# Performance work log

Measured on AMD Instinct MI355X. Metric: run time of the kernel, lower is better.

The kernel has to match this reference:

```python
import jax, jax.numpy as jnp
import numpy as np

N_HEAD = 16
D_HEAD = 64
D_MODEL = 1024
SCALE = 1.0 / float(D_HEAD) ** 0.5
LN_EPS = 1e-5


def _rel_shift(x):
    # x: [b, n, i, j] -> Transformer-XL relative shift
    b, n, i, j = x.shape
    x = jnp.pad(x, ((0, 0), (0, 0), (0, 0), (1, 0)))  # zero-pad front of last dim
    x = x.reshape(b, n, j + 1, i)[:, :, 1:, :]
    return x.reshape(b, n, i, j)


def _layer_norm(x, g, b):
    mu = jnp.mean(x, axis=-1, keepdims=True)
    var = jnp.mean(jnp.square(x - mu), axis=-1, keepdims=True)
    return g * (x - mu) / jnp.sqrt(var + LN_EPS) + b


def setup_inputs() -> dict:
    key = jax.random.key(0)
    ks = jax.random.split(key, 8)
    qlen, bsz = 1024, 4
    w = jax.random.normal(ks[0], (qlen, bsz, D_MODEL), jnp.float32)
    r = jax.random.normal(ks[1], (qlen, D_MODEL), jnp.float32)
    r_w_bias = 0.02 * jax.random.normal(ks[2], (N_HEAD, D_HEAD), jnp.float32)
    r_r_bias = 0.02 * jax.random.normal(ks[3], (N_HEAD, D_HEAD), jnp.float32)
    attn_mask = jnp.triu(jnp.ones((qlen, qlen), bool), 1)  # causal, True = masked
    qkv_w = 0.02 * jax.random.normal(ks[4], (D_MODEL, 3 * N_HEAD * D_HEAD), jnp.float32)
    qkv_b = jnp.zeros((3 * N_HEAD * D_HEAD,), jnp.float32)
    rk_w = 0.02 * jax.random.normal(ks[5], (D_MODEL, N_HEAD * D_HEAD), jnp.float32)
    rk_b = jnp.zeros((N_HEAD * D_HEAD,), jnp.float32)
    o_w = 0.02 * jax.random.normal(ks[6], (N_HEAD * D_HEAD, D_MODEL), jnp.float32)
    o_b = jnp.zeros((D_MODEL,), jnp.float32)
    ln_g = jnp.ones((D_MODEL,), jnp.float32)
    ln_b = jnp.zeros((D_MODEL,), jnp.float32)
    return {"w": w, "r": r, "r_w_bias": r_w_bias, "r_r_bias": r_r_bias,
            "qkv_w": qkv_w, "qkv_b": qkv_b, "rk_w": rk_w, "rk_b": rk_b,
            "o_w": o_w, "o_b": o_b, "ln_g": ln_g, "ln_b": ln_b,
            "attn_mask": attn_mask}


def reference(w, r, r_w_bias, r_r_bias, qkv_w, qkv_b, rk_w, rk_b, o_w, o_b, ln_g, ln_b, attn_mask):
    qlen, bsz, _ = w.shape
    # post-lnorm path (pre_lnorm=False)
    heads = w @ qkv_w + qkv_b                       # [q, b, 3*H*D]
    q, k, v = jnp.split(heads, 3, axis=-1)
    q = q.reshape(qlen, bsz, N_HEAD, D_HEAD)
    k = k.reshape(qlen, bsz, N_HEAD, D_HEAD)
    v = v.reshape(qlen, bsz, N_HEAD, D_HEAD)
    rk = (r @ rk_w + rk_b).reshape(-1, N_HEAD, D_HEAD)  # [rlen, H, D]
    AC = jnp.einsum('ibnd,jbnd->bnij', q + r_w_bias, k)
    BD = _rel_shift(jnp.einsum('ibnd,jnd->bnij', q + r_r_bias, rk))
    score = SCALE * (AC + BD)                       # [b, H, q, k]
    score = jnp.where(attn_mask[None, None, :, :], -jnp.inf, score)
    prob = jax.nn.softmax(score, axis=-1)
    vec = jnp.einsum('bnij,jbnd->ibnd', prob, v).reshape(qlen, bsz, N_HEAD * D_HEAD)
    attn_out = vec @ o_w + o_b
    return _layer_norm(w + attn_out, ln_g, ln_b)
```

## Files before the change

kernel.cpp:

```cpp
#include <hip/hip_runtime.h>
#include <math.h>

#define QL 1024
#define BSZ 4
#define NH 16
#define DH 64
#define DM 1024
#define SCALE_F 0.125f

typedef __attribute__((ext_vector_type(8))) short bf16x8;
typedef __attribute__((ext_vector_type(4))) float f32x4;

__device__ __forceinline__ unsigned short f2bf(float f) {
  union { float f; unsigned int u; } c; c.f = f;
  unsigned int u = c.u;
  u += 0x7FFFu + ((u >> 16) & 1u);
  return (unsigned short)(u >> 16);
}
__device__ __forceinline__ float bf2f(unsigned short u) {
  union { unsigned int i; float f; } c; c.i = ((unsigned int)u) << 16;
  return c.f;
}

__device__ __forceinline__ void ld_lds16(const unsigned short* g, unsigned short* l) {
  __builtin_amdgcn_global_load_lds(
      (const __attribute__((address_space(1))) unsigned int*)g,
      (__attribute__((address_space(3))) unsigned int*)l, 16, 0, 0);
}

__device__ __forceinline__ bf16x8 frag64(const unsigned short* lds, int n, int s) {
  return *(const bf16x8*)(lds + n * 64 + ((s ^ (n & 7)) * 8));
}

template <int CTRL>
__device__ __forceinline__ float dpp_mv(float x) {
  return __int_as_float(__builtin_amdgcn_update_dpp(
      0, __float_as_int(x), CTRL, 0xf, 0xf, true));
}
__device__ __forceinline__ float rowsum16(float x) {
  x += dpp_mv<0x121>(x);
  x += dpp_mv<0x122>(x);
  x += dpp_mv<0x124>(x);
  x += dpp_mv<0x128>(x);
  return x;
}

template <int R>
__device__ __forceinline__ float rot_band(float x, int quad) {
  float t0 = dpp_mv<0x121 + R>(x);
  float t1 = dpp_mv<0x124>(t0);
  float t2 = dpp_mv<0x128>(t0);
  float t3 = dpp_mv<0x12C>(t0);
  float a = (quad & 1) ? t1 : t0;
  float b = (quad & 1) ? t3 : t2;
  return (quad & 2) ? b : a;
}

__global__ __launch_bounds__(256) void prep_kernel(
    const float* __restrict__ w, const float* __restrict__ r,
    const float* __restrict__ qkv_w, const float* __restrict__ rk_w,
    const float* __restrict__ o_w,
    unsigned short* __restrict__ wb, unsigned short* __restrict__ rb,
    unsigned short* __restrict__ qkv_wt, unsigned short* __restrict__ rk_wt,
    unsigned short* __restrict__ o_wt, float* __restrict__ drk) {
  __shared__ __align__(16) unsigned short t[64][72];
  const int bid = blockIdx.x, tid = threadIdx.x;
  if (bid >= 3840) {
    int idx = (bid - 3840) * 256 + tid;
    ((float4*)drk)[idx] = make_float4(0.f, 0.f, 0.f, 0.f);
    return;
  }
  if (bid < 2560) {
    const float* in = (bid < 2048) ? w : r;
    unsigned short* out = (bid < 2048) ? wb : rb;
    int idx = ((bid < 2048) ? bid : (bid - 2048)) * 256 + tid;
    float4 a = *(const float4*)(in + (size_t)idx * 8);
    float4 b = *(const float4*)(in + (size_t)idx * 8 + 4);
    unsigned short o[8] = {f2bf(a.x), f2bf(a.y), f2bf(a.z), f2bf(a.w),
                           f2bf(b.x), f2bf(b.y), f2bf(b.z), f2bf(b.w)};
    *(uint4*)(out + (size_t)idx * 8) = *(const uint4*)o;
    return;
  }
  const float* in; unsigned short* out; int N, n0, k0;
  if (bid < 3328) {
    int l = bid - 2560; in = qkv_w; out = qkv_wt; N = 3072;
    n0 = (l % 48) * 64; k0 = (l / 48) * 64;
  } else if (bid < 3584) {
    int l = bid - 3328; in = rk_w; out = rk_wt; N = 1024;
    n0 = (l & 15) * 64; k0 = (l >> 4) * 64;
  } else {
    int l = bid - 3584; in = o_w; out = o_wt; N = 1024;
    n0 = (l & 15) * 64; k0 = (l >> 4) * 64;
  }
  for (int f = tid; f < 1024; f += 256) {
    int rr = f >> 4, c4 = (f & 15) * 4;
    float4 v = *(const float4*)(in + (size_t)(k0 + rr) * N + n0 + c4);
    t[c4 + 0][rr] = f2bf(v.x); t[c4 + 1][rr] = f2bf(v.y);
    t[c4 + 2][rr] = f2bf(v.z); t[c4 + 3][rr] = f2bf(v.w);
  }
  __syncthreads();
  for (int f = tid; f < 512; f += 256) {
    int rr = f >> 3, seg = (f & 7) * 8;
    *(uint4*)(out + (size_t)(n0 + rr) * 1024 + k0 + seg) = *(const uint4*)&t[rr][seg];
  }
}

__global__ __launch_bounds__(512) void gemm12(
    const unsigned short* __restrict__ wb, const unsigned short* __restrict__ rb,
    const unsigned short* __restrict__ qkv_wt, const unsigned short* __restrict__ rk_wt,
    const float* __restrict__ qkv_b, const float* __restrict__ rk_b,
    const float* __restrict__ rwb, const float* __restrict__ rrb,
    unsigned short* __restrict__ qbf, unsigned short* __restrict__ kbf,
    unsigned short* __restrict__ vtb, unsigned short* __restrict__ rkbf,
    float* __restrict__ drk) {
  __shared__ __align__(16) unsigned short As[2 * 4096];
  __shared__ __align__(16) unsigned short Bs[2 * 8192];
  const int bid = blockIdx.x, tid = threadIdx.x;
  const int w = tid >> 6, lane = tid & 63;
  const int quad = lane >> 4, l15 = lane & 15;
  const int wr = w >> 2, wc = w & 3;
  const bool job0 = bid < 384;
  const unsigned short *A, *BT;
  const float* bias;
  int bm, bn;
  if (job0) {
    A = wb; BT = qkv_wt; bias = qkv_b;
    bn = (bid % 12) * 256; bm = (bid / 12) * 128;
  } else {
    int l = bid - 384;
    A = rb; BT = rk_wt; bias = rk_b;
    bn = (l & 3) * 256; bm = (l >> 2) * 128;
  }
  const int srow = tid >> 2;
  const int sseg = (tid & 3) ^ (srow & 3);
  f32x4 acc[4][4] = {};

  auto stage = [&](int bf, int k0) {
    ld_lds16(A + (size_t)(bm + srow) * 1024 + k0 + sseg * 8, As + bf * 4096 + w * 512);
#pragma unroll
    for (int i = 0; i < 2; ++i)
      ld_lds16(BT + (size_t)(bn + i * 128 + srow) * 1024 + k0 + sseg * 8,
               Bs + bf * 8192 + i * 4096 + w * 512);
  };

  int buf = 0;
  stage(0, 0);
  for (int k0 = 0; k0 < 1024; k0 += 32) {
    __syncthreads();
    if (k0 + 32 < 1024) stage(buf ^ 1, k0 + 32);
    const unsigned short* Al = As + buf * 4096;
    const unsigned short* Bl = Bs + buf * 8192;
    const int sa = quad ^ (l15 & 3);
    bf16x8 af[4], bfr[4];
#pragma unroll
    for (int rt = 0; rt < 4; ++rt)
      af[rt] = *(const bf16x8*)&Al[(wr * 64 + rt * 16 + l15) * 32 + sa * 8];
#pragma unroll
    for (int nt = 0; nt < 4; ++nt)
      bfr[nt] = *(const bf16x8*)&Bl[(wc * 64 + nt * 16 + l15) * 32 + sa * 8];
#pragma unroll
    for (int rt = 0; rt < 4; ++rt)
#pragma unroll
      for (int nt = 0; nt < 4; ++nt)
        acc[rt][nt] = __builtin_amdgcn_mfma_f32_16x16x32_bf16(af[rt], bfr[nt], acc[rt][nt], 0, 0, 0);
    buf ^= 1;
  }

  if (job0) {
#pragma unroll
    for (int rt = 0; rt < 4; ++rt)
#pragma unroll
      for (int nt = 0; nt < 4; ++nt) {
        int gc = bn + wc * 64 + nt * 16 + l15;
        float bv = bias[gc];
        int part = gc >> 10, h = (gc >> 6) & 15, d = gc & 63;
#pragma unroll
        for (int reg = 0; reg < 4; ++reg) {
          int gr = bm + wr * 64 + rt * 16 + quad * 4 + reg;
          float val = acc[rt][nt][reg] + bv;
          int i = gr >> 2, b = gr & 3;
          if (part == 0)
            qbf[((size_t)((b * NH + h) * QL + i)) * DH + d] = f2bf(val);
          else if (part == 1)
            kbf[((size_t)((b * NH + h) * QL + i)) * DH + d] = f2bf(val);
          else
            vtb[((size_t)((b * NH + h) * DH + d)) * QL + i] = f2bf(val);
        }
      }
  } else {
    const int h = (bn + wc * 64) >> 6;
    float df[4];
#pragma unroll
    for (int nt = 0; nt < 4; ++nt) {
      int dd = nt * 16 + l15;
      df[nt] = rrb[h * DH + dd] - rwb[h * DH + dd];
    }
#pragma unroll
    for (int rt = 0; rt < 4; ++rt) {
      float s[4] = {0.f, 0.f, 0.f, 0.f};
#pragma unroll
      for (int nt = 0; nt < 4; ++nt) {
        int d = nt * 16 + l15;
        float bv = bias[h * DH + d];
#pragma unroll
        for (int reg = 0; reg < 4; ++reg) {
          int gr = bm + wr * 64 + rt * 16 + quad * 4 + reg;
          float val = acc[rt][nt][reg] + bv;
          rkbf[((size_t)(h * QL + gr)) * DH + d] = f2bf(val);
          s[reg] += val * df[nt];
        }
      }
#pragma unroll
      for (int reg = 0; reg < 4; ++reg) {
        float v = s[reg];
        v += __shfl_xor(v, 1);
        v += __shfl_xor(v, 2);
        v += __shfl_xor(v, 4);
        v += __shfl_xor(v, 8);
        if (l15 == 0) {
          int j = bm + wr * 64 + rt * 16 + quad * 4 + reg;
          atomicAdd(&drk[h * QL + j], v);
        }
      }
    }
  }
}

__global__ __launch_bounds__(512) void gemm_o(
    const unsigned short* __restrict__ A, const unsigned short* __restrict__ BT,
    const float* __restrict__ bias, float* __restrict__ Cf) {
  __shared__ __align__(16) unsigned short As[2 * 4096];
  __shared__ __align__(16) unsigned short Bs[2 * 2048];
  const int tid = threadIdx.x;
  const int w = tid >> 6, lane = tid & 63;
  const int quad = lane >> 4, l15 = lane & 15;
  const int wr = w >> 1, wc = w & 1;
  const int bm = blockIdx.y * 128, bn = blockIdx.x * 64;
  const int srow = w * 16 + (lane >> 2);
  const int sseg = (lane & 3) ^ ((lane >> 2) & 3);
  f32x4 acc[2][2] = {};

  auto stage = [&](int bf, int k0) {
    ld_lds16(A + (size_t)(bm + srow) * 1024 + k0 + sseg * 8, As + bf * 4096 + w * 512);
    if (w < 4)
      ld_lds16(BT + (size_t)(bn + srow) * 1024 + k0 + sseg * 8, Bs + bf * 2048 + w * 512);
  };

  int buf = 0;
  stage(0, 0);
  for (int k0 = 0; k0 < 1024; k0 += 32) {
    __syncthreads();
    if (k0 + 32 < 1024) stage(buf ^ 1, k0 + 32);
    const unsigned short* Al = As + buf * 4096;
    const unsigned short* Bl = Bs + buf * 2048;
    const int sa = quad ^ (l15 & 3);
    bf16x8 af[2], bfr[2];
#pragma unroll
    for (int rt = 0; rt < 2; ++rt)
      af[rt] = *(const bf16x8*)&Al[(wr * 32 + rt * 16 + l15) * 32 + sa * 8];
#pragma unroll
    for (int nt = 0; nt < 2; ++nt)
      bfr[nt] = *(const bf16x8*)&Bl[(wc * 32 + nt * 16 + l15) * 32 + sa * 8];
#pragma unroll
    for (int rt = 0; rt < 2; ++rt)
#pragma unroll
      for (int nt = 0; nt < 2; ++nt)
        acc[rt][nt] = __builtin_amdgcn_mfma_f32_16x16x32_bf16(af[rt], bfr[nt], acc[rt][nt], 0, 0, 0);
    buf ^= 1;
  }

#pragma unroll
  for (int rt = 0; rt < 2; ++rt)
#pragma unroll
    for (int nt = 0; nt < 2; ++nt) {
      int gc = bn + wc * 32 + nt * 16 + l15;
      float bv = bias[gc];
#pragma unroll
      for (int reg = 0; reg < 4; ++reg) {
        int gr = bm + wr * 32 + rt * 16 + quad * 4 + reg;
        Cf[(size_t)gr * DM + gc] = acc[rt][nt][reg] + bv;
      }
    }
}

__device__ const unsigned char ymap[16] = {15, 14, 13, 12, 8, 9, 10, 11,
                                           4, 5, 6, 7, 3, 2, 1, 0};

__global__ __launch_bounds__(256, 4) void attn_kernel(
    const unsigned short* __restrict__ qbf, const unsigned short* __restrict__ kbf,
    const unsigned short* __restrict__ vtb, const unsigned short* __restrict__ rkb,
    const float* __restrict__ drk, const float* __restrict__ rwb,
    unsigned short* __restrict__ vecb) {
  __shared__ __align__(16) unsigned short SH[20480];
  unsigned short* Ks = SH;
  unsigned short* Vs = SH + 8192;
  unsigned short* PM = SH + 16384;

  const int tid = threadIdx.x;
  const int wg = tid >> 6, lane = tid & 63;
  const int quad = lane >> 4, l15 = lane & 15;
  const int bh = blockIdx.x, b = bh >> 4, h = bh & 15;
  const int y = ymap[blockIdx.y];
  const int i0 = y * 64, tS = y, T = y + 1;

  const unsigned short* kB0 = kbf + (size_t)bh * QL * DH;
  const unsigned short* vB0 = vtb + (size_t)bh * DH * QL;
  const unsigned short* rB0 = rkb + (size_t)h * QL * DH;
  const float* drkh = drk + h * QL;
  unsigned short* pmw = PM + wg * 1024;

  const int srow8 = lane >> 3, sseg8 = lane & 7;

  bf16x8 qf[2];
  {
    int qrow = i0 + wg * 16 + l15;
    const unsigned short* qp = qbf + ((size_t)bh * QL + qrow) * DH;
#pragma unroll
    for (int s = 0; s < 2; ++s) {
      int off = s * 32 + quad * 8;
      uint4 raw = *(const uint4*)(qp + off);
      const unsigned short* ru = (const unsigned short*)&raw;
      float4 wb0 = *(const float4*)(rwb + h * DH + off);
      float4 wb1 = *(const float4*)(rwb + h * DH + off + 4);
      union { bf16x8 v; unsigned short u[8]; } qc;
      qc.u[0] = f2bf(bf2f(ru[0]) + wb0.x); qc.u[1] = f2bf(bf2f(ru[1]) + wb0.y);
      qc.u[2] = f2bf(bf2f(ru[2]) + wb0.z); qc.u[3] = f2bf(bf2f(ru[3]) + wb0.w);
      qc.u[4] = f2bf(bf2f(ru[4]) + wb1.x); qc.u[5] = f2bf(bf2f(ru[5]) + wb1.y);
      qc.u[6] = f2bf(bf2f(ru[6]) + wb1.z); qc.u[7] = f2bf(bf2f(ru[7]) + wb1.w);
      qf[s] = qc.v;
    }
  }

  auto rel_frag = [&](int gb, f32x4& c) {
    int row = min(gb + l15, QL - 1);
    const unsigned short* rp = rB0 + (size_t)row * DH;
    f32x4 a = {0.f, 0.f, 0.f, 0.f};
    a = __builtin_amdgcn_mfma_f32_16x16x32_bf16(qf[0], *(const bf16x8*)(rp + quad * 8), a, 0, 0, 0);
    a = __builtin_amdgcn_mfma_f32_16x16x32_bf16(qf[1], *(const bf16x8*)(rp + 32 + quad * 8), a, 0, 0, 0);
    float dv = drkh[row];
    a[0] += dv; a[1] += dv; a[2] += dv; a[3] += dv;
    c = a;
  };

  auto stage_tile = [&](int t, int buf) {
    const unsigned short* kb = kB0 + (size_t)(t * 64) * DH;
    const unsigned short* vb = vB0 + t * 64;
    unsigned short* kd = Ks + buf * 4096;
    unsigned short* vd = Vs + buf * 4096;
#pragma unroll
    for (int ii = 0; ii < 2; ++ii) {
      int row = wg * 16 + ii * 8 + srow8;
      int gs = sseg8 ^ (row & 7);
      ld_lds16(kb + (size_t)row * DH + gs * 8, kd + (wg * 16 + ii * 8) * 64);
      ld_lds16(vb + (size_t)row * QL + gs * 8, vd + (wg * 16 + ii * 8) * 64);
    }
  };

  float lrow[4] = {0.f, 0.f, 0.f, 0.f};
  f32x4 pv[4];
#pragma unroll
  for (int r = 0; r < 4; ++r) pv[r] = (f32x4){0.f, 0.f, 0.f, 0.f};

  f32x4 rc[5];
  {
    const int Bt0 = 1008 - i0 - 16 * wg;
#pragma unroll
    for (int f = 0; f < 5; ++f) rel_frag(Bt0 + 16 * f, rc[f]);
  }

  int buf = 0;
  stage_tile(0, 0);
  for (int t = 0; t < T; ++t) {
    __syncthreads();
    if (t + 1 < T) stage_tile(t + 1, buf ^ 1);
    const bool diag = (t == tS);
    const unsigned short* ksl = Ks + buf * 4096;
    const unsigned short* vsl = Vs + buf * 4096;

    f32x4 sacc[4];
#pragma unroll
    for (int nt = 0; nt < 4; ++nt) {
      int n = nt * 16 + l15;
      f32x4 c = {0.f, 0.f, 0.f, 0.f};
      c = __builtin_amdgcn_mfma_f32_16x16x32_bf16(qf[0], frag64(ksl, n, quad), c, 0, 0, 0);
      c = __builtin_amdgcn_mfma_f32_16x16x32_bf16(qf[1], frag64(ksl, n, 4 + quad), c, 0, 0, 0);
      sacc[nt] = c;
    }

#pragma unroll
    for (int r = 0; r < 4; ++r) {
      const int il = wg * 16 + quad * 4 + r;
      const int ls = l15 + 15 - quad * 4 - r;
      const bool lo = ls < 16;
      float rot[5];
#pragma unroll
      for (int f = 0; f < 5; ++f) {
        float x = rc[f][r];
        switch (r) {
          case 0: rot[f] = rot_band<0>(x, quad); break;
          case 1: rot[f] = rot_band<1>(x, quad); break;
          case 2: rot[f] = rot_band<2>(x, quad); break;
          default: rot[f] = rot_band<3>(x, quad); break;
        }
      }
      float psum = 0.f;
      const int prow = quad * 4 + r;
      const int psw = prow & 7;
#pragma unroll
      for (int nt = 0; nt < 4; ++nt) {
        float band = lo ? rot[nt] : rot[nt + 1];
        float s = (sacc[nt][r] + band) * SCALE_F;
        if (diag && (nt * 16 + l15) > il) s = -1e30f;
        float e = __expf(s);
        psum += e;
        int jl = nt * 16 + l15;
        pmw[prow * 64 + (((jl >> 3) ^ psw) << 3) + (jl & 7)] = f2bf(e);
      }
      lrow[r] += rowsum16(psum);
    }

    bf16x8 pf0 = frag64(pmw, l15, quad);
    bf16x8 pf1 = frag64(pmw, l15, 4 + quad);
#pragma unroll
    for (int nt = 0; nt < 4; ++nt) {
      int n = nt * 16 + l15;
      pv[nt] = __builtin_amdgcn_mfma_f32_16x16x32_bf16(pf0, frag64(vsl, n, quad), pv[nt], 0, 0, 0);
      pv[nt] = __builtin_amdgcn_mfma_f32_16x16x32_bf16(pf1, frag64(vsl, n, 4 + quad), pv[nt], 0, 0, 0);
    }

    if (t + 1 < T) {
      rc[0] = rc[4];
      const int Bt = 1008 - i0 + 64 * (t + 1) - 16 * wg;
#pragma unroll
      for (int f = 1; f < 5; ++f) rel_frag(Bt + 16 * f, rc[f]);
    }
    buf ^= 1;
  }

#pragma unroll
  for (int nt = 0; nt < 4; ++nt)
#pragma unroll
    for (int r = 0; r < 4; ++r) {
      int il = wg * 16 + quad * 4 + r;
      float val = pv[nt][r] / lrow[r];
      vecb[((size_t)((i0 + il) * BSZ + b)) * DM + h * DH + nt * 16 + l15] = f2bf(val);
    }
}

__global__ __launch_bounds__(256) void ln_kernel(
    const float* __restrict__ w, const float* __restrict__ attn,
    const float* __restrict__ g, const float* __restrict__ bta,
    float* __restrict__ out) {
  __shared__ float red[4];
  __shared__ float sval[2];
  const int row = blockIdx.x, tid = threadIdx.x;
  const float* wr = w + (size_t)row * DM;
  const float* ar = attn + (size_t)row * DM;
  float4 wv = *(const float4*)(wr + tid * 4);
  float4 av = *(const float4*)(ar + tid * 4);
  float x0 = wv.x + av.x, x1 = wv.y + av.y, x2 = wv.z + av.z, x3 = wv.w + av.w;
  float s = x0 + x1 + x2 + x3;
#pragma unroll
  for (int off = 32; off; off >>= 1) s += __shfl_down(s, off, 64);
  const int lane = tid & 63, wvi = tid >> 6;
  if (lane == 0) red[wvi] = s;
  __syncthreads();
  if (tid == 0) sval[0] = (red[0] + red[1] + red[2] + red[3]) * (1.0f / 1024.0f);
  __syncthreads();
  const float mu = sval[0];
  float d0 = x0 - mu, d1 = x1 - mu, d2 = x2 - mu, d3 = x3 - mu;
  float vs2 = d0 * d0 + d1 * d1 + d2 * d2 + d3 * d3;
#pragma unroll
  for (int off = 32; off; off >>= 1) vs2 += __shfl_down(vs2, off, 64);
  if (lane == 0) red[wvi] = vs2;
  __syncthreads();
  if (tid == 0)
    sval[1] = rsqrtf((red[0] + red[1] + red[2] + red[3]) * (1.0f / 1024.0f) + 1e-5f);
  __syncthreads();
  const float inv = sval[1];
  float4 gv = *(const float4*)(g + tid * 4);
  float4 bv = *(const float4*)(bta + tid * 4);
  float4 ov;
  ov.x = gv.x * d0 * inv + bv.x;
  ov.y = gv.y * d1 * inv + bv.y;
  ov.z = gv.z * d2 * inv + bv.z;
  ov.w = gv.w * d3 * inv + bv.w;
  *(float4*)(out + (size_t)row * DM + tid * 4) = ov;
}

extern "C" void kernel_launch(void* const* d_in, const int* in_sizes, int n_in,
                              void* d_out, int out_size, void* d_ws, size_t ws_size,
                              hipStream_t stream) {
  const float* w     = (const float*)d_in[0];
  const float* r     = (const float*)d_in[1];
  const float* rwb   = (const float*)d_in[2];
  const float* rrb   = (const float*)d_in[3];
  const float* qkv_w = (const float*)d_in[4];
  const float* qkv_b = (const float*)d_in[5];
  const float* rk_w  = (const float*)d_in[6];
  const float* rk_b  = (const float*)d_in[7];
  const float* o_w   = (const float*)d_in[8];
  const float* o_b   = (const float*)d_in[9];
  const float* ln_g  = (const float*)d_in[10];
  const float* ln_b  = (const float*)d_in[11];

  float* out = (float*)d_out;
  char* p = (char*)d_ws;
  unsigned short* wb     = (unsigned short*)p; p += (size_t)4096 * 1024 * 2;
  unsigned short* rb     = (unsigned short*)p; p += (size_t)1024 * 1024 * 2;
  unsigned short* qkv_wt = (unsigned short*)p; p += (size_t)3072 * 1024 * 2;
  unsigned short* rk_wt  = (unsigned short*)p; p += (size_t)1024 * 1024 * 2;
  unsigned short* o_wt   = (unsigned short*)p; p += (size_t)1024 * 1024 * 2;
  unsigned short* qbf    = (unsigned short*)p; p += (size_t)BSZ * NH * QL * DH * 2;
  unsigned short* kbf    = (unsigned short*)p; p += (size_t)BSZ * NH * QL * DH * 2;
  unsigned short* vtb    = (unsigned short*)p; p += (size_t)BSZ * NH * QL * DH * 2;
  unsigned short* rkbf   = (unsigned short*)p; p += (size_t)NH * QL * DH * 2;
  float*          drk    = (float*)p;          p += (size_t)NH * QL * 4;
  unsigned short* vecb   = (unsigned short*)p; p += (size_t)4096 * 1024 * 2;
  float*          attnf  = (float*)p;          p += (size_t)4096 * 1024 * 4;

  prep_kernel<<<3856, 256, 0, stream>>>(w, r, qkv_w, rk_w, o_w,
                                        wb, rb, qkv_wt, rk_wt, o_wt, drk);
  gemm12<<<416, 512, 0, stream>>>(wb, rb, qkv_wt, rk_wt, qkv_b, rk_b, rwb, rrb,
                                  qbf, kbf, vtb, rkbf, drk);
  attn_kernel<<<dim3(64, 16), 256, 0, stream>>>(qbf, kbf, vtb, rkbf, drk, rwb, vecb);
  gemm_o<<<dim3(16, 32), 512, 0, stream>>>(vecb, o_wt, o_b, attnf);
  ln_kernel<<<4096, 256, 0, stream>>>(w, attnf, ln_g, ln_b, out);
}
```

Baseline: 266.1 us.

## Split attention KV loop across two wave teams per block with LDS merge

Each attention block now runs 512 threads as two teams of four waves, each handling half of the causal key tiles for the same 64 query rows. The teams use separate K/V double buffers, and their partial P·V accumulators and row sums are merged through LDS before normalization. Because the softmax here uses no running max, the partial sums can simply be added. This shortens the serial tile chain for long-causal blocks, at the cost of double the LDS per block, lower occupancy, and an extra reduction step. The ymap block ordering is replaced with a plain reverse order.

```diff
diff --git a/kernel.cpp b/kernel.cpp
--- a/kernel.cpp
+++ b/kernel.cpp
@@ -283,37 +283,38 @@
     }
 }
 
-__device__ const unsigned char ymap[16] = {15, 14, 13, 12, 8, 9, 10, 11,
-                                           4, 5, 6, 7, 3, 2, 1, 0};
-
-__global__ __launch_bounds__(256, 4) void attn_kernel(
+__global__ __launch_bounds__(512, 4) void attn_kernel(
     const unsigned short* __restrict__ qbf, const unsigned short* __restrict__ kbf,
     const unsigned short* __restrict__ vtb, const unsigned short* __restrict__ rkb,
     const float* __restrict__ drk, const float* __restrict__ rwb,
     unsigned short* __restrict__ vecb) {
-  __shared__ __align__(16) unsigned short SH[20480];
-  unsigned short* Ks = SH;
-  unsigned short* Vs = SH + 8192;
-  unsigned short* PM = SH + 16384;
-
+  __shared__ __align__(16) unsigned short SH[40960];
   const int tid = threadIdx.x;
   const int wg = tid >> 6, lane = tid & 63;
+  const int team = wg >> 2, wgl = wg & 3;
   const int quad = lane >> 4, l15 = lane & 15;
   const int bh = blockIdx.x, b = bh >> 4, h = bh & 15;
-  const int y = ymap[blockIdx.y];
+  const int y = 15 - (int)blockIdx.y;
   const int i0 = y * 64, tS = y, T = y + 1;
+  const int h0 = (T + 1) >> 1;
+  const int tBeg = team ? h0 : 0;
+  const int tEnd = team ? T : h0;
+
+  unsigned short* Ks = SH + team * 16384;
+  unsigned short* Vs = Ks + 8192;
+  unsigned short* PM = SH + 32768;
+  unsigned short* pmw = PM + wg * 1024;
 
   const unsigned short* kB0 = kbf + (size_t)bh * QL * DH;
   const unsigned short* vB0 = vtb + (size_t)bh * DH * QL;
   const unsigned short* rB0 = rkb + (size_t)h * QL * DH;
   const float* drkh = drk + h * QL;
-  unsigned short* pmw = PM + wg * 1024;
 
   const int srow8 = lane >> 3, sseg8 = lane & 7;
 
   bf16x8 qf[2];
   {
-    int qrow = i0 + wg * 16 + l15;
+    int qrow = i0 + wgl * 16 + l15;
     const unsigned short* qp = qbf + ((size_t)bh * QL + qrow) * DH;
 #pragma unroll
     for (int s = 0; s < 2; ++s) {
@@ -349,10 +350,10 @@
     unsigned short* vd = Vs + buf * 4096;
 #pragma unroll
     for (int ii = 0; ii < 2; ++ii) {
-      int row = wg * 16 + ii * 8 + srow8;
+      int row = wgl * 16 + ii * 8 + srow8;
       int gs = sseg8 ^ (row & 7);
-      ld_lds16(kb + (size_t)row * DH + gs * 8, kd + (wg * 16 + ii * 8) * 64);
-      ld_lds16(vb + (size_t)row * QL + gs * 8, vd + (wg * 16 + ii * 8) * 64);
+      ld_lds16(kb + (size_t)row * DH + gs * 8, kd + (wgl * 16 + ii * 8) * 64);
+      ld_lds16(vb + (size_t)row * QL + gs * 8, vd + (wgl * 16 + ii * 8) * 64);
     }
   };
 
@@ -362,89 +363,112 @@
   for (int r = 0; r < 4; ++r) pv[r] = (f32x4){0.f, 0.f, 0.f, 0.f};
 
   f32x4 rc[5];
-  {
-    const int Bt0 = 1008 - i0 - 16 * wg;
+  if (tBeg < tEnd) {
+    const int Bt0 = 1008 - i0 + 64 * tBeg - 16 * wgl;
 #pragma unroll
     for (int f = 0; f < 5; ++f) rel_frag(Bt0 + 16 * f, rc[f]);
   }
 
   int buf = 0;
-  stage_tile(0, 0);
-  for (int t = 0; t < T; ++t) {
+  if (tBeg < tEnd) stage_tile(tBeg, 0);
+  for (int rr = 0; rr < h0; ++rr) {
     __syncthreads();
-    if (t + 1 < T) stage_tile(t + 1, buf ^ 1);
-    const bool diag = (t == tS);
-    const unsigned short* ksl = Ks + buf * 4096;
-    const unsigned short* vsl = Vs + buf * 4096;
-
-    f32x4 sacc[4];
-#pragma unroll
-    for (int nt = 0; nt < 4; ++nt) {
-      int n = nt * 16 + l15;
-      f32x4 c = {0.f, 0.f, 0.f, 0.f};
-      c = __builtin_amdgcn_mfma_f32_16x16x32_bf16(qf[0], frag64(ksl, n, quad), c, 0, 0, 0);
-      c = __builtin_amdgcn_mfma_f32_16x16x32_bf16(qf[1], frag64(ksl, n, 4 + quad), c, 0, 0, 0);
-      sacc[nt] = c;
-    }
-
-#pragma unroll
-    for (int r = 0; r < 4; ++r) {
-      const int il = wg * 16 + quad * 4 + r;
-      const int ls = l15 + 15 - quad * 4 - r;
-      const bool lo = ls < 16;
-      float rot[5];
-#pragma unroll
-      for (int f = 0; f < 5; ++f) {
-        float x = rc[f][r];
-        switch (r) {
-          case 0: rot[f] = rot_band<0>(x, quad); break;
-          case 1: rot[f] = rot_band<1>(x, quad); break;
-          case 2: rot[f] = rot_band<2>(x, quad); break;
-          default: rot[f] = rot_band<3>(x, quad); break;
+    const int t = tBeg + rr;
+    const bool act = t < tEnd;
+    if (act && t + 1 < tEnd) stage_tile(t + 1, buf ^ 1);
+    if (act) {
+      const bool diag = (t == tS);
+      const unsigned short* ksl = Ks + buf * 4096;
+      const unsigned short* vsl = Vs + buf * 4096;
+
+      f32x4 sacc[4];
+#pragma unroll
+      for (int nt = 0; nt < 4; ++nt) {
+        int n = nt * 16 + l15;
+        f32x4 c = {0.f, 0.f, 0.f, 0.f};
+        c = __builtin_amdgcn_mfma_f32_16x16x32_bf16(qf[0], frag64(ksl, n, quad), c, 0, 0, 0);
+        c = __builtin_amdgcn_mfma_f32_16x16x32_bf16(qf[1], frag64(ksl, n, 4 + quad), c, 0, 0, 0);
+        sacc[nt] = c;
+      }
+
+#pragma unroll
+      for (int r = 0; r < 4; ++r) {
+        const int il = wgl * 16 + quad * 4 + r;
+        const int ls = l15 + 15 - quad * 4 - r;
+        const bool lo = ls < 16;
+        float rot[5];
+#pragma unroll
+        for (int f = 0; f < 5; ++f) {
+          float x = rc[f][r];
+          switch (r) {
+            case 0: rot[f] = rot_band<0>(x, quad); break;
+            case 1: rot[f] = rot_band<1>(x, quad); break;
+            case 2: rot[f] = rot_band<2>(x, quad); break;
+            default: rot[f] = rot_band<3>(x, quad); break;
+          }
         }
-      }
-      float psum = 0.f;
-      const int prow = quad * 4 + r;
-      const int psw = prow & 7;
+        float psum = 0.f;
+        const int prow = quad * 4 + r;
+        const int psw = prow & 7;
+#pragma unroll
+        for (int nt = 0; nt < 4; ++nt) {
+          float band = lo ? rot[nt] : rot[nt + 1];
+          float s = (sacc[nt][r] + band) * SCALE_F;
+          if (diag && (nt * 16 + l15) > il) s = -1e30f;
+          float e = __expf(s);
+          psum += e;
+          int jl = nt * 16 + l15;
+          pmw[prow * 64 + (((jl >> 3) ^ psw) << 3) + (jl & 7)] = f2bf(e);
+        }
+        lrow[r] += rowsum16(psum);
+      }
+
+      bf16x8 pf0 = frag64(pmw, l15, quad);
+      bf16x8 pf1 = frag64(pmw, l15, 4 + quad);
 #pragma unroll
       for (int nt = 0; nt < 4; ++nt) {
-        float band = lo ? rot[nt] : rot[nt + 1];
-        float s = (sacc[nt][r] + band) * SCALE_F;
-        if (diag && (nt * 16 + l15) > il) s = -1e30f;
-        float e = __expf(s);
-        psum += e;
-        int jl = nt * 16 + l15;
-        pmw[prow * 64 + (((jl >> 3) ^ psw) << 3) + (jl & 7)] = f2bf(e);
-      }
-      lrow[r] += rowsum16(psum);
-    }
-
-    bf16x8 pf0 = frag64(pmw, l15, quad);
-    bf16x8 pf1 = frag64(pmw, l15, 4 + quad);
-#pragma unroll
-    for (int nt = 0; nt < 4; ++nt) {
-      int n = nt * 16 + l15;
-      pv[nt] = __builtin_amdgcn_mfma_f32_16x16x32_bf16(pf0, frag64(vsl, n, quad), pv[nt], 0, 0, 0);
-      pv[nt] = __builtin_amdgcn_mfma_f32_16x16x32_bf16(pf1, frag64(vsl, n, 4 + quad), pv[nt], 0, 0, 0);
-    }
-
-    if (t + 1 < T) {
-      rc[0] = rc[4];
-      const int Bt = 1008 - i0 + 64 * (t + 1) - 16 * wg;
-#pragma unroll
-      for (int f = 1; f < 5; ++f) rel_frag(Bt + 16 * f, rc[f]);
+        int n = nt * 16 + l15;
+        pv[nt] = __builtin_amdgcn_mfma_f32_16x16x32_bf16(pf0, frag64(vsl, n, quad), pv[nt], 0, 0, 0);
+        pv[nt] = __builtin_amdgcn_mfma_f32_16x16x32_bf16(pf1, frag64(vsl, n, 4 + quad), pv[nt], 0, 0, 0);
+      }
+
+      if (t + 1 < tEnd) {
+        rc[0] = rc[4];
+        const int Bt = 1008 - i0 + 64 * (t + 1) - 16 * wgl;
+#pragma unroll
+        for (int f = 1; f < 5; ++f) rel_frag(Bt + 16 * f, rc[f]);
+      }
     }
     buf ^= 1;
   }
 
-#pragma unroll
-  for (int nt = 0; nt < 4; ++nt)
-#pragma unroll
-    for (int r = 0; r < 4; ++r) {
-      int il = wg * 16 + quad * 4 + r;
-      float val = pv[nt][r] / lrow[r];
-      vecb[((size_t)((i0 + il) * BSZ + b)) * DM + h * DH + nt * 16 + l15] = f2bf(val);
-    }
+  __syncthreads();
+  if (team == 1) {
+    float* pvs = (float*)PM + wgl * 1024;
+    float* lrs = (float*)SH + wgl * 256;
+#pragma unroll
+    for (int nt = 0; nt < 4; ++nt)
+#pragma unroll
+      for (int r = 0; r < 4; ++r) pvs[(nt * 4 + r) * 64 + lane] = pv[nt][r];
+#pragma unroll
+    for (int r = 0; r < 4; ++r) lrs[r * 64 + lane] = lrow[r];
+  }
+  __syncthreads();
+  if (team == 0) {
+    const float* pvs = (const float*)PM + wgl * 1024;
+    const float* lrs = (const float*)SH + wgl * 256;
+    float linv[4];
+#pragma unroll
+    for (int r = 0; r < 4; ++r) linv[r] = 1.0f / (lrow[r] + lrs[r * 64 + lane]);
+#pragma unroll
+    for (int nt = 0; nt < 4; ++nt)
+#pragma unroll
+      for (int r = 0; r < 4; ++r) {
+        int il = wgl * 16 + quad * 4 + r;
+        float val = (pv[nt][r] + pvs[(nt * 4 + r) * 64 + lane]) * linv[r];
+        vecb[((size_t)((i0 + il) * BSZ + b)) * DM + h * DH + nt * 16 + l15] = f2bf(val);
+      }
+  }
 }
 
 __global__ __launch_bounds__(256) void ln_kernel(
@@ -523,7 +547,7 @@
                                         wb, rb, qkv_wt, rk_wt, o_wt, drk);
   gemm12<<<416, 512, 0, stream>>>(wb, rb, qkv_wt, rk_wt, qkv_b, rk_b, rwb, rrb,
                                   qbf, kbf, vtb, rkbf, drk);
-  attn_kernel<<<dim3(64, 16), 256, 0, stream>>>(qbf, kbf, vtb, rkbf, drk, rwb, vecb);
+  attn_kernel<<<dim3(64, 16), 512, 0, stream>>>(qbf, kbf, vtb, rkbf, drk, rwb, vecb);
   gemm_o<<<dim3(16, 32), 512, 0, stream>>>(vecb, o_wt, o_b, attnf);
   ln_kernel<<<4096, 256, 0, stream>>>(w, attnf, ln_g, ln_b, out);
 }
```

Result: faster. 260.5 us, median of 2 (-2.1%).
